# Optimization experiments

Hardware: AMD Instinct MI355X
Metric: run time of the kernel (lower is better)

The kernel has to match this reference:

```python
import jax, jax.numpy as jnp
import numpy as np

H = 500      # hidden size of RNNCell
D_IN = 512   # VGG16 feature channels
D_OUT = 100  # output vocab/logit dim
STEPS = 49   # 7x7 spatial grid consumed sequentially


def setup_inputs() -> dict:
    key = jax.random.key(0)
    ks = jax.random.split(key, 8)
    # post-VGG16 feature map for one 224x224 image: [1, 512, 7, 7]
    x = jax.random.normal(ks[0], (1, D_IN, 7, 7), dtype=jnp.float32)
    # original code uses torch.rand for the initial hidden state
    hidden0 = jax.random.uniform(ks[1], (1, H), dtype=jnp.float32)
    # nn.RNNCell(512, 500) params, PyTorch layout: W_ih [H, D_IN], W_hh [H, H]
    s_rnn = 1.0 / np.sqrt(H)
    W_ih = jax.random.uniform(ks[2], (H, D_IN), minval=-s_rnn, maxval=s_rnn, dtype=jnp.float32)
    W_hh = jax.random.uniform(ks[3], (H, H), minval=-s_rnn, maxval=s_rnn, dtype=jnp.float32)
    b_ih = jax.random.uniform(ks[4], (H,), minval=-s_rnn, maxval=s_rnn, dtype=jnp.float32)
    b_hh = jax.random.uniform(ks[5], (H,), minval=-s_rnn, maxval=s_rnn, dtype=jnp.float32)
    # nn.Linear(500, 100): W_out [D_OUT, H]
    s_out = 1.0 / np.sqrt(H)
    W_out = jax.random.uniform(ks[6], (D_OUT, H), minval=-s_out, maxval=s_out, dtype=jnp.float32)
    b_out = jax.random.uniform(ks[7], (D_OUT,), minval=-s_out, maxval=s_out, dtype=jnp.float32)
    return {"x": x, "hidden0": hidden0, "W_ih": W_ih, "W_hh": W_hh,
            "b_ih": b_ih, "b_hh": b_hh, "W_out": W_out, "b_out": b_out}


def reference(x, hidden0, W_ih, W_hh, b_ih, b_hh, W_out, b_out):
    # x: [1, 512, 7, 7] -> permute(0,2,3,1) -> [1,7,7,512] -> view(49, 1, 512)
    seq = jnp.transpose(x, (0, 2, 3, 1)).reshape(STEPS, 1, D_IN)
    # Precompute the input projection for all steps in one GEMM: [49, 1, H]
    xproj = jnp.einsum('tbd,hd->tbh', seq, W_ih) + b_ih + b_hh

    def step(h, xp):
        # h: [1, H]; RNNCell: h' = tanh(x W_ih^T + b_ih + h W_hh^T + b_hh)
        h = jnp.tanh(xp + h @ W_hh.T)
        out = jnp.tanh(h @ W_out.T + b_out)  # [1, D_OUT]
        return h, out

    _, outs = jax.lax.scan(step, hidden0, xproj)  # outs: [49, 1, 100]
    # torch.stack(op, 0).squeeze().unsqueeze(0) -> [1, 49, 100]
    return outs.squeeze(1)[None, :, :]
```

## Files before the change

kernel.cpp:

```cpp
#include <hip/hip_runtime.h>
#include <hip/hip_bf16.h>

#define H 500
#define D_IN 512
#define D_OUT 100
#define STEPS 49
#define NWG 4
#define SENT 0xFFFFFFFFu

typedef _Float16 h2_t __attribute__((ext_vector_type(2)));

#if defined(__has_builtin)
#if __has_builtin(__builtin_amdgcn_fdot2)
#define HAVE_FDOT2 1
#endif
#endif

__device__ __forceinline__ float fdot2f(h2_t a, h2_t b, float c) {
#ifdef HAVE_FDOT2
    return __builtin_amdgcn_fdot2(a, b, c, false);
#else
    return c + (float)a[0] * (float)b[0] + (float)a[1] * (float)b[1];
#endif
}
__device__ __forceinline__ h2_t bch2(unsigned u) { return __builtin_bit_cast(h2_t, u); }
__device__ __forceinline__ unsigned pk(float a, float b) {
    return __builtin_bit_cast(unsigned, h2_t{(_Float16)a, (_Float16)b});
}
__device__ __forceinline__ float tanh_fast(float x) {
    const float e = __expf(2.f * x);
    return 1.f - 2.f / (e + 1.f);
}
__device__ __forceinline__ int clen(int g) { return (g < 3) ? 128 : (H - 384); }

__global__ void __launch_bounds__(512, 1)
k1_xproj(const float* __restrict__ x, const float* __restrict__ W_ih,
         const float* __restrict__ b_ih, const float* __restrict__ b_hh,
         float* __restrict__ xproj, float* __restrict__ part) {
    if (blockIdx.x >= 63) {
        const int b = blockIdx.x - 63;
        float4* p4 = (float4*)part;
        const float4 s4 = {__builtin_bit_cast(float, SENT), __builtin_bit_cast(float, SENT),
                           __builtin_bit_cast(float, SENT), __builtin_bit_cast(float, SENT)};
        const int i0 = b * 1024 + threadIdx.x;
        const int i1 = i0 + 512;
        if (i0 < 25088) p4[i0] = s4;
        if (i1 < 25088) p4[i1] = s4;
        return;
    }
    __shared__ float xl[D_IN * STEPS];
    const int tid = threadIdx.x;
    for (int i = tid; i < D_IN * STEPS; i += 512) xl[i] = x[i];
    __syncthreads();

    const int wv = tid >> 6, lane = tid & 63;
    const int r = blockIdx.x * 8 + wv;
    if (r >= H) return;
    float wr8[8];
#pragma unroll
    for (int k = 0; k < 8; k++) wr8[k] = W_ih[r * D_IN + k * 64 + lane];
    float p[STEPS];
#pragma unroll
    for (int t = 0; t < STEPS; t++) p[t] = 0.f;
#pragma unroll
    for (int k = 0; k < 8; k++) {
        const float* xr = xl + (k * 64 + lane) * STEPS;
#pragma unroll
        for (int t = 0; t < STEPS; t++) p[t] = fmaf(wr8[k], xr[t], p[t]);
    }
#pragma unroll
    for (int t = 0; t < STEPS; t++) {
        float v = p[t];
        v += __shfl_xor(v, 32); v += __shfl_xor(v, 16); v += __shfl_xor(v, 8);
        v += __shfl_xor(v, 4);  v += __shfl_xor(v, 2);  v += __shfl_xor(v, 1);
        p[t] = v;
    }
    if (lane == 0) {
        const float b = b_ih[r] + b_hh[r];
        for (int t = 0; t < STEPS; t++) xproj[t * 512 + r] = p[t] + b;
    }
}

__global__ void __launch_bounds__(512, 1)
k2_scan(const float* __restrict__ hidden0, const float* __restrict__ W_hh,
        const float* __restrict__ xproj, float* part, float* __restrict__ Hs) {
    __shared__ uint4 wl[16 * 512];
    __shared__ __align__(16) _Float16 hch[2][128];

    const int g = blockIdx.x, tid = threadIdx.x;
    const int rr = tid >> 2, sub = tid & 3;
    const int myLen = clen(g);

#pragma unroll
    for (int d = 0; d < 4; d++) {
        uint4 u[4] = {{0,0,0,0},{0,0,0,0},{0,0,0,0},{0,0,0,0}};
        if (rr < clen(d)) {
            const int row = 128 * d + rr;
            const float* rowp = W_hh + (size_t)row * H + 128 * g + 32 * sub;
            const int cmax = myLen - 32 * sub;
            if (cmax >= 32) {
#pragma unroll
                for (int q8 = 0; q8 < 4; q8++) {
                    const float4 f0 = *(const float4*)(rowp + 8 * q8);
                    const float4 f1 = *(const float4*)(rowp + 8 * q8 + 4);
                    u[q8].x = pk(f0.x, f0.y); u[q8].y = pk(f0.z, f0.w);
                    u[q8].z = pk(f1.x, f1.y); u[q8].w = pk(f1.z, f1.w);
                }
            } else {
                float f[32];
#pragma unroll
                for (int cc = 0; cc < 32; cc++) f[cc] = (cc < cmax) ? rowp[cc] : 0.f;
#pragma unroll
                for (int q8 = 0; q8 < 4; q8++) {
                    u[q8].x = pk(f[8*q8+0], f[8*q8+1]);
                    u[q8].y = pk(f[8*q8+2], f[8*q8+3]);
                    u[q8].z = pk(f[8*q8+4], f[8*q8+5]);
                    u[q8].w = pk(f[8*q8+6], f[8*q8+7]);
                }
            }
        }
#pragma unroll
        for (int c = 0; c < 4; c++) wl[(d * 4 + c) * 512 + tid] = u[c];
    }
    if (tid < 128) hch[0][tid] = (tid < myLen) ? (_Float16)hidden0[128 * g + tid]
                                               : (_Float16)0.f;
    else if (tid < 256) hch[1][tid - 128] = (_Float16)0.f;
    __syncthreads();

#pragma unroll 1
    for (int t = 0; t < STEPS; ++t) {
        const int cur = t & 1;
        float xp = 0.f;
        if (sub == 0 && rr < myLen) xp = xproj[t * 512 + 128 * g + rr];

        const uint4* hc = (const uint4*)&hch[cur][0];
        uint4 hv4[4];
#pragma unroll
        for (int c = 0; c < 4; c++) hv4[c] = hc[sub * 4 + c];

        float own = 0.f;
#pragma unroll
        for (int k = 0; k < 4; k++) {
            const int d = (g + 1 + k) & 3;
            float s = 0.f;
#pragma unroll
            for (int c = 0; c < 4; c++) {
                const uint4 w = wl[(d * 4 + c) * 512 + tid];
                const uint4 hb = hv4[c];
                s = fdot2f(bch2(w.x), bch2(hb.x), s);
                s = fdot2f(bch2(w.y), bch2(hb.y), s);
                s = fdot2f(bch2(w.z), bch2(hb.z), s);
                s = fdot2f(bch2(w.w), bch2(hb.w), s);
            }
            s += __shfl_xor(s, 1);
            s += __shfl_xor(s, 2);
            if (k < 3) {
                if (sub == 0)
                    __hip_atomic_store(&part[((t * 4 + d) * 4 + g) * 128 + rr], s,
                                       __ATOMIC_RELAXED, __HIP_MEMORY_SCOPE_AGENT);
            } else own = s;
        }

        if (sub == 0 && rr < myLen) {
            const int g1 = (g + 1) & 3, g2 = (g + 2) & 3, g3 = (g + 3) & 3;
            const float* pb = &part[(t * 4 + g) * 4 * 128];
            unsigned b1 = SENT, b2 = SENT, b3 = SENT;
            do {
                if (b1 == SENT) b1 = __builtin_bit_cast(unsigned,
                    __hip_atomic_load(&pb[g1 * 128 + rr], __ATOMIC_RELAXED,
                                      __HIP_MEMORY_SCOPE_AGENT));
                if (b2 == SENT) b2 = __builtin_bit_cast(unsigned,
                    __hip_atomic_load(&pb[g2 * 128 + rr], __ATOMIC_RELAXED,
                                      __HIP_MEMORY_SCOPE_AGENT));
                if (b3 == SENT) b3 = __builtin_bit_cast(unsigned,
                    __hip_atomic_load(&pb[g3 * 128 + rr], __ATOMIC_RELAXED,
                                      __HIP_MEMORY_SCOPE_AGENT));
            } while (b1 == SENT || b2 == SENT || b3 == SENT);
            const float tot = own + __builtin_bit_cast(float, b1)
                                  + __builtin_bit_cast(float, b2)
                                  + __builtin_bit_cast(float, b3) + xp;
            const float hv = tanh_fast(tot);
            Hs[t * 512 + 128 * g + rr] = hv;
            hch[cur ^ 1][rr] = (_Float16)hv;
        }
        __syncthreads();
    }
}

__global__ void k3_out(const float* __restrict__ Hs, const float* __restrict__ W_out,
                       const float* __restrict__ b_out, float* __restrict__ out) {
    const int t = blockIdx.x, o = threadIdx.x;
    if (o < D_OUT) {
        const float4* wr = (const float4*)(W_out + o * H);
        const float4* hr = (const float4*)(Hs + t * 512);
        float acc = b_out[o];
#pragma unroll 5
        for (int i = 0; i < 125; i++) {
            const float4 wv = wr[i];
            const float4 hv = hr[i];
            acc = fmaf(wv.x, hv.x, acc);
            acc = fmaf(wv.y, hv.y, acc);
            acc = fmaf(wv.z, hv.z, acc);
            acc = fmaf(wv.w, hv.w, acc);
        }
        out[t * D_OUT + o] = tanh_fast(acc);
    }
}

extern "C" void kernel_launch(void* const* d_in, const int* in_sizes, int n_in,
                              void* d_out, int out_size, void* d_ws, size_t ws_size,
                              hipStream_t stream) {
    const float* x       = (const float*)d_in[0];
    const float* hidden0 = (const float*)d_in[1];
    const float* W_ih    = (const float*)d_in[2];
    const float* W_hh    = (const float*)d_in[3];
    const float* b_ih    = (const float*)d_in[4];
    const float* b_hh    = (const float*)d_in[5];
    const float* W_out   = (const float*)d_in[6];
    const float* b_out   = (const float*)d_in[7];
    float* out = (float*)d_out;

    char* ws = (char*)d_ws;
    float* part  = (float*)ws;
    float* xproj = (float*)(ws + 401408);
    float* Hs    = (float*)(ws + 501760);

    k1_xproj<<<88, 512, 0, stream>>>(x, W_ih, b_ih, b_hh, xproj, part);
    k2_scan<<<NWG, 512, 0, stream>>>(hidden0, W_hh, xproj, part, Hs);
    k3_out<<<STEPS, 128, 0, stream>>>(Hs, W_out, b_out, out);
}
```

Before: 100.2 us.

## Co-locate scan workgroups on one XCD and poll partial sums via L2

Launches 48 workgroups for the scan and elects the first XCD that collects four of them. Those four run the recurrence and the rest exit, so the cross-workgroup partial-sum exchange stays within one XCD's L2. Polling switches to inline-asm sc0 loads of all three partials at once, with a spin limit that falls back to agent-scope atomic loads. It risks visibility and correctness problems if the L2-scoped loads do not see stores from other XCDs, plus extra launch and election overhead.

```diff
diff --git a/kernel.cpp b/kernel.cpp
--- a/kernel.cpp
+++ b/kernel.cpp
@@ -6,6 +6,8 @@
 #define D_OUT 100
 #define STEPS 49
 #define NWG 4
+#define NBLK2 48
+#define SPINL 240
 #define SENT 0xFFFFFFFFu
 
 typedef _Float16 h2_t __attribute__((ext_vector_type(2)));
@@ -32,13 +34,30 @@
     return 1.f - 2.f / (e + 1.f);
 }
 __device__ __forceinline__ int clen(int g) { return (g < 3) ? 128 : (H - 384); }
+__device__ __forceinline__ unsigned aload(const float* p) {
+    return __builtin_bit_cast(unsigned,
+        __hip_atomic_load(p, __ATOMIC_RELAXED, __HIP_MEMORY_SCOPE_AGENT));
+}
+__device__ __forceinline__ void astore(float* p, float v) {
+    __hip_atomic_store(p, v, __ATOMIC_RELAXED, __HIP_MEMORY_SCOPE_AGENT);
+}
+__device__ __forceinline__ void l2load3(const float* p1, const float* p2, const float* p3,
+                                        unsigned& a, unsigned& b, unsigned& c) {
+    asm volatile("global_load_dword %0, %3, off sc0\n\t"
+                 "global_load_dword %1, %4, off sc0\n\t"
+                 "global_load_dword %2, %5, off sc0\n\t"
+                 "s_waitcnt vmcnt(0)"
+                 : "=&v"(a), "=&v"(b), "=&v"(c)
+                 : "v"(p1), "v"(p2), "v"(p3));
+}
 
 __global__ void __launch_bounds__(512, 1)
 k1_xproj(const float* __restrict__ x, const float* __restrict__ W_ih,
          const float* __restrict__ b_ih, const float* __restrict__ b_hh,
-         float* __restrict__ xproj, float* __restrict__ part) {
+         float* __restrict__ xproj, float* __restrict__ part, unsigned* __restrict__ elect) {
     if (blockIdx.x >= 63) {
         const int b = blockIdx.x - 63;
+        if (b == 0 && threadIdx.x < 16) elect[threadIdx.x] = 0u;
         float4* p4 = (float4*)part;
         const float4 s4 = {__builtin_bit_cast(float, SENT), __builtin_bit_cast(float, SENT),
                            __builtin_bit_cast(float, SENT), __builtin_bit_cast(float, SENT)};
@@ -83,11 +102,36 @@
 
 __global__ void __launch_bounds__(512, 1)
 k2_scan(const float* __restrict__ hidden0, const float* __restrict__ W_hh,
-        const float* __restrict__ xproj, float* part, float* __restrict__ Hs) {
+        const float* __restrict__ xproj, float* part, float* __restrict__ Hs,
+        unsigned* elect) {
     __shared__ uint4 wl[16 * 512];
     __shared__ __align__(16) _Float16 hch[2][128];
-
-    const int g = blockIdx.x, tid = threadIdx.x;
+    __shared__ unsigned role_s[2];
+
+    const int tid = threadIdx.x;
+
+    if (tid == 0) {
+        unsigned xcd;
+        asm volatile("s_getreg_b32 %0, hwreg(HW_REG_XCC_ID)" : "=s"(xcd));
+        xcd &= 7u;
+        const unsigned ticket = __hip_atomic_fetch_add(&elect[xcd], 1u,
+                                    __ATOMIC_RELAXED, __HIP_MEMORY_SCOPE_AGENT);
+        if (ticket == 3u) {
+            unsigned exp0 = 0u;
+            __hip_atomic_compare_exchange_strong(&elect[8], &exp0, xcd + 1u,
+                __ATOMIC_RELAXED, __ATOMIC_RELAXED, __HIP_MEMORY_SCOPE_AGENT);
+        }
+        unsigned win;
+        do {
+            win = __hip_atomic_load(&elect[8], __ATOMIC_RELAXED, __HIP_MEMORY_SCOPE_AGENT);
+        } while (win == 0u);
+        role_s[0] = (win == xcd + 1u && ticket < 4u) ? 1u : 0u;
+        role_s[1] = ticket;
+    }
+    __syncthreads();
+    if (role_s[0] == 0u) return;
+    const int g = (int)role_s[1];
+
     const int rr = tid >> 2, sub = tid & 3;
     const int myLen = clen(g);
 
@@ -127,6 +171,7 @@
     else if (tid < 256) hch[1][tid - 128] = (_Float16)0.f;
     __syncthreads();
 
+    bool fb = false;
 #pragma unroll 1
     for (int t = 0; t < STEPS; ++t) {
         const int cur = t & 1;
@@ -155,27 +200,36 @@
             s += __shfl_xor(s, 1);
             s += __shfl_xor(s, 2);
             if (k < 3) {
-                if (sub == 0)
-                    __hip_atomic_store(&part[((t * 4 + d) * 4 + g) * 128 + rr], s,
-                                       __ATOMIC_RELAXED, __HIP_MEMORY_SCOPE_AGENT);
+                if (sub == 0) {
+                    float* dst = &part[((t * 4 + d) * 4 + g) * 128 + rr];
+                    *dst = s;
+                    astore(dst, s);
+                }
             } else own = s;
         }
 
         if (sub == 0 && rr < myLen) {
             const int g1 = (g + 1) & 3, g2 = (g + 2) & 3, g3 = (g + 3) & 3;
             const float* pb = &part[(t * 4 + g) * 4 * 128];
+            const float* p1 = &pb[g1 * 128 + rr];
+            const float* p2 = &pb[g2 * 128 + rr];
+            const float* p3 = &pb[g3 * 128 + rr];
             unsigned b1 = SENT, b2 = SENT, b3 = SENT;
-            do {
-                if (b1 == SENT) b1 = __builtin_bit_cast(unsigned,
-                    __hip_atomic_load(&pb[g1 * 128 + rr], __ATOMIC_RELAXED,
-                                      __HIP_MEMORY_SCOPE_AGENT));
-                if (b2 == SENT) b2 = __builtin_bit_cast(unsigned,
-                    __hip_atomic_load(&pb[g2 * 128 + rr], __ATOMIC_RELAXED,
-                                      __HIP_MEMORY_SCOPE_AGENT));
-                if (b3 == SENT) b3 = __builtin_bit_cast(unsigned,
-                    __hip_atomic_load(&pb[g3 * 128 + rr], __ATOMIC_RELAXED,
-                                      __HIP_MEMORY_SCOPE_AGENT));
-            } while (b1 == SENT || b2 == SENT || b3 == SENT);
+            if (!fb) {
+                int spins = 0;
+                for (;;) {
+                    l2load3(p1, p2, p3, b1, b2, b3);
+                    if (b1 != SENT && b2 != SENT && b3 != SENT) break;
+                    if (++spins >= SPINL) { fb = true; break; }
+                }
+            }
+            if (b1 == SENT || b2 == SENT || b3 == SENT) {
+                do {
+                    if (b1 == SENT) b1 = aload(p1);
+                    if (b2 == SENT) b2 = aload(p2);
+                    if (b3 == SENT) b3 = aload(p3);
+                } while (b1 == SENT || b2 == SENT || b3 == SENT);
+            }
             const float tot = own + __builtin_bit_cast(float, b1)
                                   + __builtin_bit_cast(float, b2)
                                   + __builtin_bit_cast(float, b3) + xp;
@@ -221,11 +275,12 @@
     float* out = (float*)d_out;
 
     char* ws = (char*)d_ws;
-    float* part  = (float*)ws;
-    float* xproj = (float*)(ws + 401408);
-    float* Hs    = (float*)(ws + 501760);
-
-    k1_xproj<<<88, 512, 0, stream>>>(x, W_ih, b_ih, b_hh, xproj, part);
-    k2_scan<<<NWG, 512, 0, stream>>>(hidden0, W_hh, xproj, part, Hs);
+    float*    part  = (float*)ws;
+    float*    xproj = (float*)(ws + 401408);
+    float*    Hs    = (float*)(ws + 501760);
+    unsigned* elect = (unsigned*)(ws + 602112);
+
+    k1_xproj<<<88, 512, 0, stream>>>(x, W_ih, b_ih, b_hh, xproj, part, elect);
+    k2_scan<<<NBLK2, 512, 0, stream>>>(hidden0, W_hh, xproj, part, Hs, elect);
     k3_out<<<STEPS, 128, 0, stream>>>(Hs, W_out, b_out, out);
 }
```

Measured after the change: 130.9 us. 30.6% more time.

## Split recurrent scan over eight workgroups and fuse output projection into scan kernel

Applied to the files above, without the earlier changes.

The recurrent W_hh matvec is now split across eight workgroups of 64 hidden units instead of four of 128, so each thread does one uint4 of fp16 dot work per partner chunk and the per-step dot-product latency drops. The k3 output kernel is removed: after the scan, each workgroup computes the output projection for a strided subset of timesteps, reading Hs behind sentinel-based readiness polling. Hs stores are deferred by one step and written atomically, and the sentinel region grows to cover Hs. In exchange each step now waits on seven cross-workgroup partials instead of three, which adds global-memory synchronisation traffic.

```diff
diff --git a/kernel.cpp b/kernel.cpp
--- a/kernel.cpp
+++ b/kernel.cpp
@@ -5,7 +5,7 @@
 #define D_IN 512
 #define D_OUT 100
 #define STEPS 49
-#define NWG 4
+#define NWG 8
 #define SENT 0xFFFFFFFFu
 
 typedef _Float16 h2_t __attribute__((ext_vector_type(2)));
@@ -31,21 +31,30 @@
     const float e = __expf(2.f * x);
     return 1.f - 2.f / (e + 1.f);
 }
-__device__ __forceinline__ int clen(int g) { return (g < 3) ? 128 : (H - 384); }
+__device__ __forceinline__ int clen(int g) { return (g < 7) ? 64 : (H - 448); }
+__device__ __forceinline__ unsigned aload(const float* p) {
+    return __builtin_bit_cast(unsigned,
+        __hip_atomic_load(p, __ATOMIC_RELAXED, __HIP_MEMORY_SCOPE_AGENT));
+}
+__device__ __forceinline__ void astore(float* p, float v) {
+    __hip_atomic_store(p, v, __ATOMIC_RELAXED, __HIP_MEMORY_SCOPE_AGENT);
+}
 
 __global__ void __launch_bounds__(512, 1)
 k1_xproj(const float* __restrict__ x, const float* __restrict__ W_ih,
          const float* __restrict__ b_ih, const float* __restrict__ b_hh,
-         float* __restrict__ xproj, float* __restrict__ part) {
+         float* __restrict__ xproj, float* __restrict__ sentreg) {
     if (blockIdx.x >= 63) {
         const int b = blockIdx.x - 63;
-        float4* p4 = (float4*)part;
+        float4* p4 = (float4*)sentreg;
         const float4 s4 = {__builtin_bit_cast(float, SENT), __builtin_bit_cast(float, SENT),
                            __builtin_bit_cast(float, SENT), __builtin_bit_cast(float, SENT)};
-        const int i0 = b * 1024 + threadIdx.x;
-        const int i1 = i0 + 512;
-        if (i0 < 25088) p4[i0] = s4;
-        if (i1 < 25088) p4[i1] = s4;
+        const int base = b * 512 + (int)threadIdx.x;
+#pragma unroll
+        for (int j = 0; j < 4; j++) {
+            const int idx = j * 12800 + base;
+            if (idx < 50176) p4[idx] = s4;
+        }
         return;
     }
     __shared__ float xl[D_IN * STEPS];
@@ -83,127 +92,117 @@
 
 __global__ void __launch_bounds__(512, 1)
 k2_scan(const float* __restrict__ hidden0, const float* __restrict__ W_hh,
-        const float* __restrict__ xproj, float* part, float* __restrict__ Hs) {
-    __shared__ uint4 wl[16 * 512];
-    __shared__ __align__(16) _Float16 hch[2][128];
+        const float* __restrict__ xproj, float* part, float* Hs,
+        const float* __restrict__ W_out, const float* __restrict__ b_out,
+        float* __restrict__ out) {
+    __shared__ uint4 wl[NWG * 512];
+    __shared__ __align__(16) _Float16 hch[2][64];
 
     const int g = blockIdx.x, tid = threadIdx.x;
-    const int rr = tid >> 2, sub = tid & 3;
+    const int rr = tid >> 3, sub = tid & 7;
     const int myLen = clen(g);
-
-#pragma unroll
-    for (int d = 0; d < 4; d++) {
-        uint4 u[4] = {{0,0,0,0},{0,0,0,0},{0,0,0,0},{0,0,0,0}};
-        if (rr < clen(d)) {
-            const int row = 128 * d + rr;
-            const float* rowp = W_hh + (size_t)row * H + 128 * g + 32 * sub;
-            const int cmax = myLen - 32 * sub;
-            if (cmax >= 32) {
-#pragma unroll
-                for (int q8 = 0; q8 < 4; q8++) {
-                    const float4 f0 = *(const float4*)(rowp + 8 * q8);
-                    const float4 f1 = *(const float4*)(rowp + 8 * q8 + 4);
-                    u[q8].x = pk(f0.x, f0.y); u[q8].y = pk(f0.z, f0.w);
-                    u[q8].z = pk(f1.x, f1.y); u[q8].w = pk(f1.z, f1.w);
-                }
-            } else {
-                float f[32];
-#pragma unroll
-                for (int cc = 0; cc < 32; cc++) f[cc] = (cc < cmax) ? rowp[cc] : 0.f;
-#pragma unroll
-                for (int q8 = 0; q8 < 4; q8++) {
-                    u[q8].x = pk(f[8*q8+0], f[8*q8+1]);
-                    u[q8].y = pk(f[8*q8+2], f[8*q8+3]);
-                    u[q8].z = pk(f[8*q8+4], f[8*q8+5]);
-                    u[q8].w = pk(f[8*q8+6], f[8*q8+7]);
-                }
+    const bool epi = (sub == 0) && (rr < myLen);
+
+#pragma unroll
+    for (int d = 0; d < NWG; d++) {
+        uint4 u = {0u, 0u, 0u, 0u};
+        const int row = 64 * d + rr;
+        if (row < H) {
+            const float* rowp = W_hh + (size_t)row * H + 64 * g + 8 * sub;
+            const int cmax = (H - 64 * g) - 8 * sub;
+            if (cmax >= 8) {
+                const float4 f0 = *(const float4*)(rowp);
+                const float4 f1 = *(const float4*)(rowp + 4);
+                u.x = pk(f0.x, f0.y); u.y = pk(f0.z, f0.w);
+                u.z = pk(f1.x, f1.y); u.w = pk(f1.z, f1.w);
+            } else if (cmax > 0) {
+                float f[8];
+#pragma unroll
+                for (int cc = 0; cc < 8; cc++) f[cc] = (cc < cmax) ? rowp[cc] : 0.f;
+                u.x = pk(f[0], f[1]); u.y = pk(f[2], f[3]);
+                u.z = pk(f[4], f[5]); u.w = pk(f[6], f[7]);
             }
         }
-#pragma unroll
-        for (int c = 0; c < 4; c++) wl[(d * 4 + c) * 512 + tid] = u[c];
-    }
-    if (tid < 128) hch[0][tid] = (tid < myLen) ? (_Float16)hidden0[128 * g + tid]
-                                               : (_Float16)0.f;
-    else if (tid < 256) hch[1][tid - 128] = (_Float16)0.f;
+        wl[d * 512 + tid] = u;
+    }
+    if (tid < 64) hch[0][tid] = (tid < myLen) ? (_Float16)hidden0[64 * g + tid]
+                                              : (_Float16)0.f;
+    else if (tid < 128) hch[1][tid - 64] = (_Float16)0.f;
     __syncthreads();
 
+    float prevHv = 0.f;
 #pragma unroll 1
     for (int t = 0; t < STEPS; ++t) {
         const int cur = t & 1;
+        if (t > 0 && epi) astore(&Hs[(t - 1) * 512 + 64 * g + rr], prevHv);
         float xp = 0.f;
-        if (sub == 0 && rr < myLen) xp = xproj[t * 512 + 128 * g + rr];
-
-        const uint4* hc = (const uint4*)&hch[cur][0];
-        uint4 hv4[4];
-#pragma unroll
-        for (int c = 0; c < 4; c++) hv4[c] = hc[sub * 4 + c];
-
+        if (epi) xp = xproj[t * 512 + 64 * g + rr];
+
+        const uint4 hb = ((const uint4*)&hch[cur][0])[sub];
         float own = 0.f;
 #pragma unroll
-        for (int k = 0; k < 4; k++) {
-            const int d = (g + 1 + k) & 3;
-            float s = 0.f;
-#pragma unroll
-            for (int c = 0; c < 4; c++) {
-                const uint4 w = wl[(d * 4 + c) * 512 + tid];
-                const uint4 hb = hv4[c];
-                s = fdot2f(bch2(w.x), bch2(hb.x), s);
-                s = fdot2f(bch2(w.y), bch2(hb.y), s);
-                s = fdot2f(bch2(w.z), bch2(hb.z), s);
-                s = fdot2f(bch2(w.w), bch2(hb.w), s);
-            }
+        for (int k = 0; k < 8; k++) {
+            const int d = (g + 1 + k) & 7;
+            const uint4 w = wl[d * 512 + tid];
+            float s = fdot2f(bch2(w.x), bch2(hb.x), 0.f);
+            s = fdot2f(bch2(w.y), bch2(hb.y), s);
+            s = fdot2f(bch2(w.z), bch2(hb.z), s);
+            s = fdot2f(bch2(w.w), bch2(hb.w), s);
             s += __shfl_xor(s, 1);
             s += __shfl_xor(s, 2);
-            if (k < 3) {
+            s += __shfl_xor(s, 4);
+            if (k < 7) {
                 if (sub == 0)
-                    __hip_atomic_store(&part[((t * 4 + d) * 4 + g) * 128 + rr], s,
-                                       __ATOMIC_RELAXED, __HIP_MEMORY_SCOPE_AGENT);
+                    astore(&part[((t * 8 + d) * 7 + (6 - k)) * 64 + rr], s);
             } else own = s;
         }
 
-        if (sub == 0 && rr < myLen) {
-            const int g1 = (g + 1) & 3, g2 = (g + 2) & 3, g3 = (g + 3) & 3;
-            const float* pb = &part[(t * 4 + g) * 4 * 128];
-            unsigned b1 = SENT, b2 = SENT, b3 = SENT;
+        if (epi) {
+            const float* pb = &part[(t * 8 + g) * 7 * 64];
+            unsigned bb[7];
+#pragma unroll
+            for (int j = 0; j < 7; j++) bb[j] = SENT;
+            bool all;
             do {
-                if (b1 == SENT) b1 = __builtin_bit_cast(unsigned,
-                    __hip_atomic_load(&pb[g1 * 128 + rr], __ATOMIC_RELAXED,
-                                      __HIP_MEMORY_SCOPE_AGENT));
-                if (b2 == SENT) b2 = __builtin_bit_cast(unsigned,
-                    __hip_atomic_load(&pb[g2 * 128 + rr], __ATOMIC_RELAXED,
-                                      __HIP_MEMORY_SCOPE_AGENT));
-                if (b3 == SENT) b3 = __builtin_bit_cast(unsigned,
-                    __hip_atomic_load(&pb[g3 * 128 + rr], __ATOMIC_RELAXED,
-                                      __HIP_MEMORY_SCOPE_AGENT));
-            } while (b1 == SENT || b2 == SENT || b3 == SENT);
-            const float tot = own + __builtin_bit_cast(float, b1)
-                                  + __builtin_bit_cast(float, b2)
-                                  + __builtin_bit_cast(float, b3) + xp;
+                all = true;
+#pragma unroll
+                for (int j = 0; j < 7; j++)
+                    if (bb[j] == SENT) {
+                        bb[j] = aload(&pb[j * 64 + rr]);
+                        if (bb[j] == SENT) all = false;
+                    }
+            } while (!all);
+            float tot = own + xp;
+#pragma unroll
+            for (int j = 0; j < 7; j++) tot += __builtin_bit_cast(float, bb[j]);
             const float hv = tanh_fast(tot);
-            Hs[t * 512 + 128 * g + rr] = hv;
+            prevHv = hv;
             hch[cur ^ 1][rr] = (_Float16)hv;
         }
         __syncthreads();
     }
-}
-
-__global__ void k3_out(const float* __restrict__ Hs, const float* __restrict__ W_out,
-                       const float* __restrict__ b_out, float* __restrict__ out) {
-    const int t = blockIdx.x, o = threadIdx.x;
-    if (o < D_OUT) {
-        const float4* wr = (const float4*)(W_out + o * H);
-        const float4* hr = (const float4*)(Hs + t * 512);
-        float acc = b_out[o];
+    if (epi) astore(&Hs[(STEPS - 1) * 512 + 64 * g + rr], prevHv);
+
+    float* hsm = (float*)wl;
+    for (int tt = g; tt < STEPS; tt += NWG) {
+        if (tid < H) {
+            unsigned hb2 = aload(&Hs[tt * 512 + tid]);
+            while (hb2 == SENT) hb2 = aload(&Hs[tt * 512 + tid]);
+            hsm[tid] = __builtin_bit_cast(float, hb2);
+        }
+        __syncthreads();
+        const int o = tid >> 2, q4 = tid & 3;
+        if (o < D_OUT) {
+            float s = 0.f;
+            const float* wr_ = W_out + o * H + q4;
+            const float* hr_ = hsm + q4;
 #pragma unroll 5
-        for (int i = 0; i < 125; i++) {
-            const float4 wv = wr[i];
-            const float4 hv = hr[i];
-            acc = fmaf(wv.x, hv.x, acc);
-            acc = fmaf(wv.y, hv.y, acc);
-            acc = fmaf(wv.z, hv.z, acc);
-            acc = fmaf(wv.w, hv.w, acc);
-        }
-        out[t * D_OUT + o] = tanh_fast(acc);
+            for (int j = 0; j < 125; j++) s = fmaf(wr_[4 * j], hr_[4 * j], s);
+            s += __shfl_xor(s, 1);
+            s += __shfl_xor(s, 2);
+            if (q4 == 0) out[tt * D_OUT + o] = tanh_fast(s + b_out[o]);
+        }
+        __syncthreads();
     }
 }
 
@@ -222,10 +221,9 @@
 
     char* ws = (char*)d_ws;
     float* part  = (float*)ws;
-    float* xproj = (float*)(ws + 401408);
-    float* Hs    = (float*)(ws + 501760);
-
-    k1_xproj<<<88, 512, 0, stream>>>(x, W_ih, b_ih, b_hh, xproj, part);
-    k2_scan<<<NWG, 512, 0, stream>>>(hidden0, W_hh, xproj, part, Hs);
-    k3_out<<<STEPS, 128, 0, stream>>>(Hs, W_out, b_out, out);
-}
+    float* Hs    = (float*)(ws + 702464);
+    float* xproj = (float*)(ws + 802816);
+
+    k1_xproj<<<88, 512, 0, stream>>>(x, W_ih, b_ih, b_hh, xproj, part );
+    k2_scan<<<NWG, 512, 0, stream>>>(hidden0, W_hh, xproj, part, Hs, W_out, b_out, out);
+}
```

New measurement: 225.9 us. 125% more time.
